# Performance work log

Measured on AMD Instinct MI355X. Metric: run time of the kernel, lower is better.

The kernel has to match this reference:

```python
import jax, jax.numpy as jnp
import numpy as np

DIM = 768
NUM_HEADS = 12
HEAD_DIM = DIM // NUM_HEADS
SCALE = HEAD_DIM ** -0.5


def setup_inputs() -> dict:
    key = jax.random.key(0)
    k1, k2, k3 = jax.random.split(key, 3)
    B, N = 4, 2048
    x = jax.random.normal(k1, (B, N, DIM), dtype=jnp.float32)
    Wqkv = jax.random.normal(k2, (DIM, 3 * DIM), dtype=jnp.float32) * (DIM ** -0.5)
    Wproj = jax.random.normal(k3, (DIM, DIM), dtype=jnp.float32) * (DIM ** -0.5)
    bproj = jnp.zeros((DIM,), dtype=jnp.float32)
    return {"x": x, "Wqkv": Wqkv, "Wproj": Wproj, "bproj": bproj}


def reference(x, Wqkv, Wproj, bproj):
    B, N, C = x.shape
    # qkv: [B, N, 3, H, D] -> split into q, k, v each [B, H, N, D]
    qkv = (x @ Wqkv).reshape(B, N, 3, NUM_HEADS, HEAD_DIM)
    qkv = jnp.transpose(qkv, (2, 0, 3, 1, 4))
    q, k, v = qkv[0], qkv[1], qkv[2]
    attn = jnp.einsum("bhnd,bhmd->bhnm", q, k) * SCALE
    attn = jax.nn.softmax(attn, axis=-1)  # dropout p=0 -> identity
    out = jnp.einsum("bhnm,bhmd->bhnd", attn, v)
    out = jnp.transpose(out, (0, 2, 1, 3)).reshape(B, N, C)
    return out @ Wproj + bproj
```

## Files before the change

kernel.cpp:

```cpp
#include <hip/hip_runtime.h>
#include <math.h>

typedef __bf16 bf16;
typedef __attribute__((ext_vector_type(8))) __bf16 bf16x8;
typedef __attribute__((ext_vector_type(4))) __bf16 bf16x4;
typedef __attribute__((ext_vector_type(4))) float f32x4;

#define NHEADS 12
#define HDIM 64
#define BATCH 4
#define SEQ 2048
#define CDIM 768
#define MTOK (BATCH * SEQ)
#define PERPART ((size_t)MTOK * CDIM)
#define NBH (BATCH * NHEADS)
#define NKB (SEQ / 64)

#define KSCALE 0.18033688011112042f
#define SHIFT 11.54156032f

__device__ static inline void load_lds_16(const void* g, void* l)
{
    __builtin_amdgcn_global_load_lds(
        (const __attribute__((address_space(1))) unsigned int*)g,
        (__attribute__((address_space(3))) unsigned int*)l, 16, 0, 0);
}

__global__ __launch_bounds__(256)
void prep(const float* __restrict__ x, const float* __restrict__ Wqkv,
          const float* __restrict__ Wproj,
          bf16* __restrict__ xb, bf16* __restrict__ wqt, bf16* __restrict__ wpt)
{
    __shared__ bf16 T[64][65];
    const int bid = blockIdx.x;
    const int t   = threadIdx.x;

    if (bid < 3072) {
        const size_t i = ((size_t)bid * 256 + t) * 8;
        const float4 v0 = *(const float4*)(x + i);
        const float4 v1 = *(const float4*)(x + i + 4);
        alignas(16) bf16 o[8];
        o[0] = (bf16)v0.x; o[1] = (bf16)v0.y; o[2] = (bf16)v0.z; o[3] = (bf16)v0.w;
        o[4] = (bf16)v1.x; o[5] = (bf16)v1.y; o[6] = (bf16)v1.z; o[7] = (bf16)v1.w;
        *(uint4*)(xb + i) = *(const uint4*)o;
        return;
    }

    const float* in; bf16* outp; int C, bx, by;
    if (bid < 3072 + 432) {
        const int b2 = bid - 3072;
        in = Wqkv; outp = wqt; C = 3 * CDIM; bx = b2 % 36; by = b2 / 36;
    } else {
        const int b2 = bid - 3504;
        in = Wproj; outp = wpt; C = CDIM;    bx = b2 % 12; by = b2 / 12;
    }
    const int r0 = by * 64, c0 = bx * 64;
    const int ir = t >> 2, ic = (t & 3) * 16;
    #pragma unroll
    for (int e = 0; e < 16; ++e)
        T[ir][ic + e] = (bf16)in[(size_t)(r0 + ir) * C + c0 + ic + e];
    __syncthreads();
    const int oc = t >> 2, orr = (t & 3) * 16;
    alignas(16) bf16 tmp[16];
    #pragma unroll
    for (int e = 0; e < 16; ++e)
        tmp[e] = T[orr + e][oc];
    bf16* dst = outp + (size_t)(c0 + oc) * CDIM + r0 + orr;
    *(uint4*)dst       = *(const uint4*)tmp;
    *(uint4*)(dst + 8) = *(const uint4*)(tmp + 8);
}

template<int NCOLS, int MODE>
__global__ __launch_bounds__(256, 3)
void gemm128(const bf16* __restrict__ A, const bf16* __restrict__ Bt,
             const float* __restrict__ bias,
             bf16* __restrict__ qb, bf16* __restrict__ kb, bf16* __restrict__ vtb,
             float* __restrict__ outf)
{
    __shared__ bf16 As[128 * 64];
    __shared__ bf16 Bs[128 * 64];

    const int t    = threadIdx.x;
    const int w    = t >> 6, lane = t & 63;
    const int ln   = lane & 15, quad = lane >> 4;
    const int wr   = w >> 1, wc = w & 1;
    const int m0   = blockIdx.x * 128, n0 = blockIdx.y * 128;

    f32x4 acc[4][4] = {};

    for (int k0 = 0; k0 < CDIM; k0 += 64) {
        #pragma unroll
        for (int i = 0; i < 4; ++i) {
            const int S   = w * 256 + i * 64 + lane;
            const int row = S >> 3, g = (S & 7) ^ (row & 7);
            load_lds_16(A  + (size_t)(m0 + row) * CDIM + k0 + g * 8,
                        &As[(w * 4 + i) * 512]);
            load_lds_16(Bt + (size_t)(n0 + row) * CDIM + k0 + g * 8,
                        &Bs[(w * 4 + i) * 512]);
        }
        __syncthreads();

        #pragma unroll
        for (int kk = 0; kk < 2; ++kk) {
            bf16x8 af[4], bf_[4];
            #pragma unroll
            for (int mt = 0; mt < 4; ++mt) {
                const int row = wr * 64 + mt * 16 + ln;
                af[mt] = *(const bf16x8*)&As[row * 64 + ((kk * 4 + quad) ^ (row & 7)) * 8];
            }
            #pragma unroll
            for (int nt = 0; nt < 4; ++nt) {
                const int row = wc * 64 + nt * 16 + ln;
                bf_[nt] = *(const bf16x8*)&Bs[row * 64 + ((kk * 4 + quad) ^ (row & 7)) * 8];
            }
            #pragma unroll
            for (int mt = 0; mt < 4; ++mt)
                #pragma unroll
                for (int nt = 0; nt < 4; ++nt)
                    acc[mt][nt] = __builtin_amdgcn_mfma_f32_16x16x32_bf16(
                        af[mt], bf_[nt], acc[mt][nt], 0, 0, 0);
        }
        __syncthreads();
    }

    #pragma unroll
    for (int nt = 0; nt < 4; ++nt) {
        const int c = n0 + wc * 64 + nt * 16 + ln;
        if constexpr (MODE == 0) {
            const int p = c / CDIM, rem = c - p * CDIM;
            const int h = rem >> 6, d = rem & 63;
            #pragma unroll
            for (int mt = 0; mt < 4; ++mt) {
                const int row0 = m0 + wr * 64 + mt * 16 + quad * 4;
                const int b = row0 >> 11, nn = row0 & 2047;
                if (p == 0) {
                    bf16* dst = qb + ((size_t)(b * NHEADS + h) * SEQ + nn) * HDIM + d;
                    #pragma unroll
                    for (int r = 0; r < 4; ++r) dst[r * HDIM] = (bf16)acc[mt][nt][r];
                } else if (p == 1) {
                    bf16* dst = kb + ((size_t)(b * NHEADS + h) * SEQ + nn) * HDIM + d;
                    #pragma unroll
                    for (int r = 0; r < 4; ++r) dst[r * HDIM] = (bf16)(acc[mt][nt][r] * KSCALE);
                } else {
                    alignas(8) bf16 pk[4];
                    #pragma unroll
                    for (int r = 0; r < 4; ++r) pk[r] = (bf16)acc[mt][nt][r];
                    const int nn2 = (nn & ~31) + ((nn >> 2) & 3) * 8 + ((nn >> 4) & 1) * 4;
                    *(uint2*)(vtb + ((size_t)(b * NHEADS + h) * HDIM + d) * SEQ + nn2) =
                        *(const uint2*)pk;
                }
            }
        } else {
            const float bv = bias[c];
            #pragma unroll
            for (int mt = 0; mt < 4; ++mt) {
                const int row0 = m0 + wr * 64 + mt * 16 + quad * 4;
                #pragma unroll
                for (int r = 0; r < 4; ++r)
                    outf[(size_t)(row0 + r) * CDIM + c] = acc[mt][nt][r] + bv;
            }
        }
    }
}

__global__ __launch_bounds__(256, 4)
void attn_kernel(const bf16* __restrict__ Qg, const bf16* __restrict__ Kg,
                 const bf16* __restrict__ Vtg, bf16* __restrict__ ao)
{
    __shared__ bf16 Ks[2][64 * 64];
    __shared__ bf16 Vs[2][64 * 64];

    const int virt = (blockIdx.x & 7) * 96 + (blockIdx.x >> 3);
    const int xq   = virt & 15;
    const int bh   = virt >> 4;

    const int t    = threadIdx.x;
    const int w    = t >> 6, lane = t & 63;
    const int ln   = lane & 15, quad = lane >> 4;
    const int q0   = xq * 128;

    const bf16* Qb = Qg  + (size_t)bh * SEQ * HDIM;
    const bf16* Kb = Kg  + (size_t)bh * SEQ * HDIM;
    const bf16* Vb = Vtg + (size_t)bh * HDIM * SEQ;

    bf16x8 qf[2][2];
    #pragma unroll
    for (int qt = 0; qt < 2; ++qt)
        #pragma unroll
        for (int kk = 0; kk < 2; ++kk) {
            const int row = w * 32 + qt * 16 + ln;
            qf[qt][kk] = *(const bf16x8*)(Qb + (size_t)(q0 + row) * HDIM
                                          + (kk * 4 + quad) * 8);
        }

    #pragma unroll
    for (int i = 0; i < 2; ++i) {
        const int S = w * 128 + i * 64 + lane;
        const int row = S >> 3, g = (S & 7) ^ (row & 7);
        load_lds_16(Kb + (size_t)row * HDIM + g * 8, &Ks[0][(w * 2 + i) * 512]);
        load_lds_16(Vb + (size_t)row * SEQ + g * 8,  &Vs[0][(w * 2 + i) * 512]);
    }
    __syncthreads();

    bf16x8 ones;
    #pragma unroll
    for (int e = 0; e < 8; ++e) ones[e] = (bf16)1.0f;

    f32x4 o_acc[2][4] = {};
    f32x4 racc[2] = {};

    for (int kb = 0; kb < NKB; ++kb) {
        if (kb + 1 < NKB) {
            const int nb   = (kb + 1) & 1;
            const int kpos = (kb + 1) * 64;
            #pragma unroll
            for (int i = 0; i < 2; ++i) {
                const int S = w * 128 + i * 64 + lane;
                const int row = S >> 3, g = (S & 7) ^ (row & 7);
                load_lds_16(Kb + (size_t)(kpos + row) * HDIM + g * 8,
                            &Ks[nb][(w * 2 + i) * 512]);
                load_lds_16(Vb + (size_t)row * SEQ + kpos + g * 8,
                            &Vs[nb][(w * 2 + i) * 512]);
            }
        }

        const bf16* Ksb = Ks[kb & 1];
        const bf16* Vsb = Vs[kb & 1];

        #pragma unroll
        for (int p = 0; p < 2; ++p) {
            union { bf16x8 v8; bf16x4 v4[2]; } pf8[2];
            #pragma unroll
            for (int sub = 0; sub < 2; ++sub) {
                const int mt = p * 2 + sub;
                bf16x8 ka[2];
                #pragma unroll
                for (int kk = 0; kk < 2; ++kk) {
                    const int row = mt * 16 + ln;
                    const int g = (kk * 4 + quad) ^ (row & 7);
                    ka[kk] = *(const bf16x8*)&Ksb[row * 64 + g * 8];
                }
                #pragma unroll
                for (int qt = 0; qt < 2; ++qt) {
                    f32x4 a = {-SHIFT, -SHIFT, -SHIFT, -SHIFT};
                    a = __builtin_amdgcn_mfma_f32_16x16x32_bf16(ka[0], qf[qt][0], a, 0, 0, 0);
                    a = __builtin_amdgcn_mfma_f32_16x16x32_bf16(ka[1], qf[qt][1], a, 0, 0, 0);
                    bf16x4 pb = { (bf16)__builtin_amdgcn_exp2f(a[0]),
                                  (bf16)__builtin_amdgcn_exp2f(a[1]),
                                  (bf16)__builtin_amdgcn_exp2f(a[2]),
                                  (bf16)__builtin_amdgcn_exp2f(a[3]) };
                    pf8[qt].v4[sub] = pb;
                }
            }
            __builtin_amdgcn_s_setprio(1);
            #pragma unroll
            for (int qt = 0; qt < 2; ++qt)
                racc[qt] = __builtin_amdgcn_mfma_f32_16x16x32_bf16(
                    pf8[qt].v8, ones, racc[qt], 0, 0, 0);
            #pragma unroll
            for (int dt = 0; dt < 4; ++dt) {
                const int row = dt * 16 + ln;
                const int g = (p * 4 + quad) ^ (row & 7);
                const bf16x8 vvv = *(const bf16x8*)&Vsb[row * 64 + g * 8];
                #pragma unroll
                for (int qt = 0; qt < 2; ++qt)
                    o_acc[qt][dt] = __builtin_amdgcn_mfma_f32_16x16x32_bf16(
                        pf8[qt].v8, vvv, o_acc[qt][dt], 0, 0, 0);
            }
            __builtin_amdgcn_s_setprio(0);
        }
        __syncthreads();
    }

    const int b = bh / NHEADS, h = bh - b * NHEADS;
    bf16* Ao = ao + (size_t)b * SEQ * CDIM + h * HDIM;
    #pragma unroll
    for (int qt = 0; qt < 2; ++qt) {
        float inv[4];
        #pragma unroll
        for (int r = 0; r < 4; ++r) inv[r] = 1.0f / racc[qt][r];
        #pragma unroll
        for (int dt = 0; dt < 4; ++dt) {
            const int d = dt * 16 + ln;
            #pragma unroll
            for (int r = 0; r < 4; ++r) {
                const int q = q0 + w * 32 + qt * 16 + quad * 4 + r;
                Ao[(size_t)q * CDIM + d] = (bf16)(o_acc[qt][dt][r] * inv[r]);
            }
        }
    }
}

extern "C" void kernel_launch(void* const* d_in, const int* in_sizes, int n_in,
                              void* d_out, int out_size, void* d_ws, size_t ws_size,
                              hipStream_t stream)
{
    const float* x     = (const float*)d_in[0];
    const float* Wqkv  = (const float*)d_in[1];
    const float* Wproj = (const float*)d_in[2];
    const float* bproj = (const float*)d_in[3];
    float* out = (float*)d_out;

    bf16* ws   = (bf16*)d_ws;
    bf16* xb   = ws;
    bf16* wqt  = xb  + PERPART;
    bf16* wpt  = wqt + (size_t)3 * CDIM * CDIM;
    bf16* q    = wpt + (size_t)CDIM * CDIM;
    bf16* k    = q   + PERPART;
    bf16* vt   = k   + PERPART;
    bf16* ao   = vt  + PERPART;

    prep<<<dim3(3072 + 432 + 144), 256, 0, stream>>>(x, Wqkv, Wproj, xb, wqt, wpt);

    gemm128<3 * CDIM, 0><<<dim3(MTOK / 128, 3 * CDIM / 128), 256, 0, stream>>>(
        xb, wqt, nullptr, q, k, vt, nullptr);
    attn_kernel<<<dim3(16 * NBH), 256, 0, stream>>>(q, k, vt, ao);
    gemm128<CDIM, 1><<<dim3(MTOK / 128, CDIM / 128), 256, 0, stream>>>(
        ao, wpt, bproj, nullptr, nullptr, nullptr, out);
}
```

Baseline: 190.9 us.

## Double-buffer GEMM LDS tiles with K-step 32 to overlap loads and MFMA

Measured after the change: 198.6 us. +4.0%, slower.

```diff
diff --git a/kernel.cpp b/kernel.cpp
--- a/kernel.cpp
+++ b/kernel.cpp
@@ -77,8 +77,8 @@
              bf16* __restrict__ qb, bf16* __restrict__ kb, bf16* __restrict__ vtb,
              float* __restrict__ outf)
 {
-    __shared__ bf16 As[128 * 64];
-    __shared__ bf16 Bs[128 * 64];
+    __shared__ bf16 As[2][128 * 32];
+    __shared__ bf16 Bs[2][128 * 32];
 
     const int t    = threadIdx.x;
     const int w    = t >> 6, lane = t & 63;
@@ -86,40 +86,54 @@
     const int wr   = w >> 1, wc = w & 1;
     const int m0   = blockIdx.x * 128, n0 = blockIdx.y * 128;
 
+    const int S0   = w * 2 * 64 + lane;
+    const int S1   = S0 + 64;
+    const int row0 = S0 >> 2, g0 = (S0 & 3) ^ (row0 & 3);
+    const int row1 = S1 >> 2, g1 = (S1 & 3) ^ (row1 & 3);
+
     f32x4 acc[4][4] = {};
 
-    for (int k0 = 0; k0 < CDIM; k0 += 64) {
-        #pragma unroll
-        for (int i = 0; i < 4; ++i) {
-            const int S   = w * 256 + i * 64 + lane;
-            const int row = S >> 3, g = (S & 7) ^ (row & 7);
-            load_lds_16(A  + (size_t)(m0 + row) * CDIM + k0 + g * 8,
-                        &As[(w * 4 + i) * 512]);
-            load_lds_16(Bt + (size_t)(n0 + row) * CDIM + k0 + g * 8,
-                        &Bs[(w * 4 + i) * 512]);
-        }
-        __syncthreads();
-
-        #pragma unroll
-        for (int kk = 0; kk < 2; ++kk) {
-            bf16x8 af[4], bf_[4];
-            #pragma unroll
-            for (int mt = 0; mt < 4; ++mt) {
-                const int row = wr * 64 + mt * 16 + ln;
-                af[mt] = *(const bf16x8*)&As[row * 64 + ((kk * 4 + quad) ^ (row & 7)) * 8];
-            }
-            #pragma unroll
-            for (int nt = 0; nt < 4; ++nt) {
-                const int row = wc * 64 + nt * 16 + ln;
-                bf_[nt] = *(const bf16x8*)&Bs[row * 64 + ((kk * 4 + quad) ^ (row & 7)) * 8];
-            }
-            #pragma unroll
-            for (int mt = 0; mt < 4; ++mt)
-                #pragma unroll
-                for (int nt = 0; nt < 4; ++nt)
-                    acc[mt][nt] = __builtin_amdgcn_mfma_f32_16x16x32_bf16(
-                        af[mt], bf_[nt], acc[mt][nt], 0, 0, 0);
-        }
+    load_lds_16(A  + (size_t)(m0 + row0) * CDIM + g0 * 8, &As[0][(w * 2) * 512]);
+    load_lds_16(Bt + (size_t)(n0 + row0) * CDIM + g0 * 8, &Bs[0][(w * 2) * 512]);
+    load_lds_16(A  + (size_t)(m0 + row1) * CDIM + g1 * 8, &As[0][(w * 2 + 1) * 512]);
+    load_lds_16(Bt + (size_t)(n0 + row1) * CDIM + g1 * 8, &Bs[0][(w * 2 + 1) * 512]);
+    __syncthreads();
+
+    const int NSTEP = CDIM / 32;
+    for (int s = 0; s < NSTEP; ++s) {
+        if (s + 1 < NSTEP) {
+            const int nb = (s + 1) & 1, k0 = (s + 1) * 32;
+            load_lds_16(A  + (size_t)(m0 + row0) * CDIM + k0 + g0 * 8,
+                        &As[nb][(w * 2) * 512]);
+            load_lds_16(Bt + (size_t)(n0 + row0) * CDIM + k0 + g0 * 8,
+                        &Bs[nb][(w * 2) * 512]);
+            load_lds_16(A  + (size_t)(m0 + row1) * CDIM + k0 + g1 * 8,
+                        &As[nb][(w * 2 + 1) * 512]);
+            load_lds_16(Bt + (size_t)(n0 + row1) * CDIM + k0 + g1 * 8,
+                        &Bs[nb][(w * 2 + 1) * 512]);
+        }
+
+        const bf16* Asb = As[s & 1];
+        const bf16* Bsb = Bs[s & 1];
+
+        bf16x8 af[4], bf_[4];
+        #pragma unroll
+        for (int mt = 0; mt < 4; ++mt) {
+            const int row = wr * 64 + mt * 16 + ln;
+            af[mt] = *(const bf16x8*)&Asb[row * 32 + (quad ^ (row & 3)) * 8];
+        }
+        #pragma unroll
+        for (int nt = 0; nt < 4; ++nt) {
+            const int row = wc * 64 + nt * 16 + ln;
+            bf_[nt] = *(const bf16x8*)&Bsb[row * 32 + (quad ^ (row & 3)) * 8];
+        }
+        #pragma unroll
+        for (int mt = 0; mt < 4; ++mt)
+            #pragma unroll
+            for (int nt = 0; nt < 4; ++nt)
+                acc[mt][nt] = __builtin_amdgcn_mfma_f32_16x16x32_bf16(
+                    af[mt], bf_[nt], acc[mt][nt], 0, 0, 0);
+
         __syncthreads();
     }
 
@@ -131,8 +145,8 @@
             const int h = rem >> 6, d = rem & 63;
             #pragma unroll
             for (int mt = 0; mt < 4; ++mt) {
-                const int row0 = m0 + wr * 64 + mt * 16 + quad * 4;
-                const int b = row0 >> 11, nn = row0 & 2047;
+                const int row0_ = m0 + wr * 64 + mt * 16 + quad * 4;
+                const int b = row0_ >> 11, nn = row0_ & 2047;
                 if (p == 0) {
                     bf16* dst = qb + ((size_t)(b * NHEADS + h) * SEQ + nn) * HDIM + d;
                     #pragma unroll
@@ -154,10 +168,10 @@
             const float bv = bias[c];
             #pragma unroll
             for (int mt = 0; mt < 4; ++mt) {
-                const int row0 = m0 + wr * 64 + mt * 16 + quad * 4;
+                const int row0_ = m0 + wr * 64 + mt * 16 + quad * 4;
                 #pragma unroll
                 for (int r = 0; r < 4; ++r)
-                    outf[(size_t)(row0 + r) * CDIM + c] = acc[mt][nt][r] + bv;
+                    outf[(size_t)(row0_ + r) * CDIM + c] = acc[mt][nt][r] + bv;
             }
         }
     }
```
